# Kernel tuning notes

Hardware: AMD Instinct MI355X
Metric: run time of the kernel (lower is better)

Reference implementation:

```python
import jax, jax.numpy as jnp
import numpy as np

DIMS = [512, 256, 256, 256, 256, 256, 128, 128, 64, 40]
N_NODES = 100000
N_EDGES = 3200000


def setup_inputs() -> dict:
    key = jax.random.key(0)
    ks = jax.random.split(key, 4 + 2 * 9)
    inp = {
        "x": jax.random.normal(ks[0], (N_NODES, DIMS[0]), dtype=jnp.float32),
        "edge_src": jax.random.randint(ks[1], (N_EDGES,), 0, N_NODES, dtype=jnp.int32),
        "edge_dst": jax.random.randint(ks[2], (N_EDGES,), 0, N_NODES, dtype=jnp.int32),
        "edge_weight": jax.random.uniform(ks[3], (N_EDGES,), dtype=jnp.float32) / 32.0,
    }
    for i in range(9):
        fi, fo = DIMS[i], DIMS[i + 1]
        scale = 1.0 / np.sqrt(fi)
        inp[f"W{i+1}"] = jax.random.normal(ks[4 + 2 * i], (fi, fo), dtype=jnp.float32) * scale
        inp[f"b{i+1}"] = jax.random.normal(ks[5 + 2 * i], (fo,), dtype=jnp.float32) * scale
    return inp


def _gcn_layer(h, W, b, src, dst, w, n_nodes):
    # support = h @ W; out[i] = sum over edges (i <- j) of w * support[j] + b
    support = h @ W                          # [N, fo]
    msgs = w[:, None] * support[src]         # [E, fo] gather
    agg = jax.ops.segment_sum(msgs, dst, num_segments=n_nodes)  # [N, fo] scatter-add
    return agg + b


def reference(x, edge_src, edge_dst, edge_weight,
              W1, b1, W2, b2, W3, b3, W4, b4, W5, b5,
              W6, b6, W7, b7, W8, b8, W9, b9):
    n = x.shape[0]
    Ws = (W1, W2, W3, W4, W5, W6, W7, W8, W9)
    bs = (b1, b2, b3, b4, b5, b6, b7, b8, b9)
    h = x
    for i in range(8):  # layers 1..8 with ReLU
        h = jax.nn.relu(_gcn_layer(h, Ws[i], bs[i], edge_src, edge_dst, edge_weight, n))
    h = _gcn_layer(h, Ws[8], bs[8], edge_src, edge_dst, edge_weight, n)
    return jax.nn.log_softmax(h, axis=1)
```

## Files before the change

### kernel.cpp

```cpp
#include <hip/hip_runtime.h>
#include <cstdint>
#include <cstddef>

typedef __attribute__((ext_vector_type(8))) short bf16x8;
typedef __attribute__((ext_vector_type(4))) float f32x4;

static inline int cdiv(int a, int b) { return (a + b - 1) / b; }

__device__ inline unsigned short f2bf(float f) {
    union { float f; unsigned int u; } v; v.f = f;
    unsigned int u = v.u;
    return (unsigned short)((u + 0x7FFFu + ((u >> 16) & 1u)) >> 16);
}
__device__ inline float bf2f(unsigned short b) {
    union { unsigned int u; float f; } v; v.u = ((unsigned int)b) << 16;
    return v.f;
}

__device__ inline void fma16(float* a, const int4& d, float ws) {
    const int dw[4] = {d.x, d.y, d.z, d.w};
#pragma unroll
    for (int w = 0; w < 4; ++w) {
        a[w * 4 + 0] += ws * (float)(char)(dw[w]);
        a[w * 4 + 1] += ws * (float)(char)(dw[w] >> 8);
        a[w * 4 + 2] += ws * (float)(char)(dw[w] >> 16);
        a[w * 4 + 3] += ws * (float)(dw[w] >> 24);
    }
}


struct TW {
    const float* W[9];
    int K[9];
    int N[9];
    int base[10];
    int nN;
};

__global__ __launch_bounds__(256) void prep_kernel(TW tw, unsigned short* __restrict__ Wt,
                                                   int* __restrict__ deg,
                                                   int* __restrict__ bucketCursor, int total) {
    int t = blockIdx.x * 256 + threadIdx.x;
    if (t < tw.nN) deg[t] = 0;
    if (t < 8) bucketCursor[t] = 0;
    if (t >= total) return;
    int l = 0;
#pragma unroll
    for (int i = 1; i <= 8; ++i)
        if (t >= tw.base[i]) l = i;
    int loc = t - tw.base[l];
    int K = tw.K[l], N = tw.N[l];
    int n = loc / K, k = loc - n * K;
    float v = (n < N) ? tw.W[l][(size_t)k * N + n] : 0.f;
    Wt[t] = f2bf(v);
}


__global__ __launch_bounds__(256) void partition_kernel(
        const int* __restrict__ src, const int* __restrict__ dst,
        const float* __restrict__ w,
        int* __restrict__ bucketCursor, int4* __restrict__ staging,
        int bucketCap, int nE, int nN) {
    __shared__ int lcount[8];
    __shared__ int lbase[8];
    int tid = threadIdx.x;
    int i = blockIdx.x * 256 + tid;
    if (tid < 8) lcount[tid] = 0;
    __syncthreads();
    int b = 0, d = 0, s = 0, lslot = 0;
    float wv = 0.f;
    bool act = (i < nE);
    if (act) {
        d = dst[i]; s = src[i]; wv = w[i];
        b = (int)(((long long)d * 8) / nN);
        lslot = atomicAdd(&lcount[b], 1);
    }
    __syncthreads();
    if (tid < 8) lbase[tid] = lcount[tid] ? atomicAdd(&bucketCursor[tid], lcount[tid]) : 0;
    __syncthreads();
    if (act) {
        int pos = lbase[b] + lslot;
        staging[(size_t)b * bucketCap + pos] = make_int4(d, s, __float_as_int(wv), 0);
    }
}


#define DC_BPB 32

__global__ __launch_bounds__(256) void deg_count(const int4* __restrict__ staging,
                                                 const int* __restrict__ bucketCnt,
                                                 int bucketCap, int* __restrict__ deg, int nN) {
    __shared__ int hist[12512];
    int bucket = blockIdx.x & 7;
    int chunk = blockIdx.x >> 3;
    int cnt = bucketCnt[bucket];
    int lo = (int)(((long long)bucket * nN + 7) / 8);
    int hi = (int)(((long long)(bucket + 1) * nN + 7) / 8);
    if (hi > nN) hi = nN;
    int span = hi - lo;
    for (int i = threadIdx.x; i < span; i += 256) hist[i] = 0;
    __syncthreads();
    const int4* st = staging + (size_t)bucket * bucketCap;
    for (int i = chunk * 256 + threadIdx.x; i < cnt; i += DC_BPB * 256)
        atomicAdd(&hist[st[i].x - lo], 1);
    __syncthreads();
    for (int i = threadIdx.x; i < span; i += 256) {
        int v = hist[i];
        if (v) atomicAdd(&deg[lo + i], v);
    }
}


__global__ __launch_bounds__(256) void scan_part(const int* __restrict__ deg,
                                                 int* __restrict__ partials, int n) {
    __shared__ int sdata[256];
    int tid = threadIdx.x;
    int base = blockIdx.x * 1024;
    int local = 0;
#pragma unroll
    for (int i = 0; i < 4; ++i) {
        int idx = base + tid * 4 + i;
        local += (idx < n) ? deg[idx] : 0;
    }
    sdata[tid] = local;
    __syncthreads();
    for (int off = 128; off; off >>= 1) {
        if (tid < off) sdata[tid] += sdata[tid + off];
        __syncthreads();
    }
    if (tid == 0) partials[blockIdx.x] = sdata[0];
}

__global__ __launch_bounds__(256) void scan_final2(const int* __restrict__ deg,
                                                   const int* __restrict__ partials,
                                                   int* __restrict__ rowptr,
                                                   int* __restrict__ cursor, int n, int nb) {
    __shared__ int ps[128];
    __shared__ int sdata[256];
    int tid = threadIdx.x;
    if (tid < 128) ps[tid] = (tid < nb) ? partials[tid] : 0;
    __syncthreads();
    for (int off = 1; off < 128; off <<= 1) {
        int t = (tid < 128 && tid >= off) ? ps[tid - off] : 0;
        __syncthreads();
        if (tid < 128) ps[tid] += t;
        __syncthreads();
    }
    int base = (blockIdx.x == 0) ? 0 : ps[blockIdx.x - 1];
    if (blockIdx.x == 0 && tid == 0) rowptr[n] = ps[nb - 1];
    int bb = blockIdx.x * 1024;
    int vals[4];
    int local = 0;
#pragma unroll
    for (int i = 0; i < 4; ++i) {
        int idx = bb + tid * 4 + i;
        vals[i] = (idx < n) ? deg[idx] : 0;
        local += vals[i];
    }
    sdata[tid] = local;
    __syncthreads();
    for (int off = 1; off < 256; off <<= 1) {
        int t = (tid >= off) ? sdata[tid - off] : 0;
        __syncthreads();
        sdata[tid] += t;
        __syncthreads();
    }
    int run = sdata[tid] - local + base;
#pragma unroll
    for (int i = 0; i < 4; ++i) {
        int idx = bb + tid * 4 + i;
        if (idx < n) { rowptr[idx] = run; cursor[idx] = run; }
        run += vals[i];
    }
}


__global__ __launch_bounds__(256) void scatter_b(const int4* __restrict__ staging,
                                                 const int* __restrict__ bucketCnt,
                                                 int bucketCap, int* __restrict__ cursor,
                                                 int2* __restrict__ ep, int blocksPerBucket) {
    int bucket = blockIdx.x & 7;
    int chunk = blockIdx.x >> 3;
    int cnt = bucketCnt[bucket];
    const int4* st = staging + (size_t)bucket * bucketCap;
    for (int i = chunk * 256 + threadIdx.x; i < cnt; i += blocksPerBucket * 256) {
        int4 r = st[i];
        int pos = atomicAdd(&cursor[r.x], 1);
        ep[pos] = make_int2(r.y, r.z);
    }
}


template <int BN, bool AF32, bool OUTQ>
__global__ __launch_bounds__(256) void gemm_mfma(const void* __restrict__ Av,
                                                 const unsigned short* __restrict__ Bt,
                                                 void* __restrict__ Cv,
                                                 float* __restrict__ scArr,
                                                 int M, int K, int N) {
    constexpr int BM = 128, BK = 64;
    __shared__ unsigned short As[BM * BK];
    __shared__ unsigned short Bs[BN * BK];
    const int tid = threadIdx.x;
    const int lane = tid & 63, wid = tid >> 6;
    const int m0 = blockIdx.x * BM, n0 = blockIdx.y * BN;

    constexpr int WN = (BN == 128) ? 2 : 1;
    constexpr int WTM = (BN == 128) ? 64 : 32;
    constexpr int FM = WTM / 16, FN = 4;
    const int wm = (wid / WN) * WTM;
    const int wn = (wid % WN) * 64;
    const int g = lane >> 4, r16 = lane & 15;

    const unsigned short* A16 = (const unsigned short*)Av;
    const float* A32 = (const float*)Av;

    f32x4 acc[FM][FN] = {};

    for (int k0 = 0; k0 < K; k0 += BK) {
        if constexpr (AF32) {
#pragma unroll
            for (int it = 0; it < 4; ++it) {
                int c = it * 256 + tid;
                int r = c >> 3, kc = c & 7;
                int gm = m0 + r;
                bf16x8 val;
                if (gm < M) {
                    const float* p = A32 + (size_t)gm * K + k0 + kc * 8;
                    float4 v0 = *reinterpret_cast<const float4*>(p);
                    float4 v1 = *reinterpret_cast<const float4*>(p + 4);
                    val[0] = (short)f2bf(v0.x); val[1] = (short)f2bf(v0.y);
                    val[2] = (short)f2bf(v0.z); val[3] = (short)f2bf(v0.w);
                    val[4] = (short)f2bf(v1.x); val[5] = (short)f2bf(v1.y);
                    val[6] = (short)f2bf(v1.z); val[7] = (short)f2bf(v1.w);
                } else {
#pragma unroll
                    for (int j = 0; j < 8; ++j) val[j] = 0;
                }
                *reinterpret_cast<bf16x8*>(&As[r * BK + kc * 8]) = val;
            }
        } else {
#pragma unroll
            for (int c = 0; c < 4; ++c) {
                int base = wid * 32 + c * 8;
                int row = base + (lane >> 3), kc = lane & 7;
                const unsigned short* gp = A16 + (size_t)(m0 + row) * K + k0 + kc * 8;
                __builtin_amdgcn_global_load_lds(
                    (const __attribute__((address_space(1))) void*)gp,
                    (__attribute__((address_space(3))) void*)&As[base * BK], 16, 0, 0);
            }
        }
        {
            constexpr int BCALLS = (BN * BK) / (512 * 4);
#pragma unroll
            for (int c = 0; c < BCALLS; ++c) {
                int base = wid * (BN / 4) + c * 8;
                int row = base + (lane >> 3), kc = lane & 7;
                const unsigned short* gp = Bt + (size_t)(n0 + row) * K + k0 + kc * 8;
                __builtin_amdgcn_global_load_lds(
                    (const __attribute__((address_space(1))) void*)gp,
                    (__attribute__((address_space(3))) void*)&Bs[base * BK], 16, 0, 0);
            }
        }
        __syncthreads();
#pragma unroll
        for (int ks = 0; ks < 2; ++ks) {
            bf16x8 af[FM], bfr[FN];
#pragma unroll
            for (int i = 0; i < FM; ++i)
                af[i] = *reinterpret_cast<const bf16x8*>(&As[(wm + i * 16 + r16) * BK + ks * 32 + g * 8]);
#pragma unroll
            for (int j = 0; j < FN; ++j)
                bfr[j] = *reinterpret_cast<const bf16x8*>(&Bs[(wn + j * 16 + r16) * BK + ks * 32 + g * 8]);
#pragma unroll
            for (int i = 0; i < FM; ++i)
#pragma unroll
                for (int j = 0; j < FN; ++j)
                    acc[i][j] = __builtin_amdgcn_mfma_f32_16x16x32_bf16(af[i], bfr[j], acc[i][j], 0, 0, 0);
        }
        __syncthreads();
    }

    if constexpr (OUTQ) {
        __shared__ float rmax2[2][BM];
        const int wc = wid % WN;
        char* C8 = (char*)Cv;
#pragma unroll
        for (int i = 0; i < FM; ++i) {
#pragma unroll
            for (int r = 0; r < 4; ++r) {
                float m = 0.f;
#pragma unroll
                for (int j = 0; j < FN; ++j) m = fmaxf(m, fabsf(acc[i][j][r]));
                m = fmaxf(m, __shfl_xor(m, 1));
                m = fmaxf(m, __shfl_xor(m, 2));
                m = fmaxf(m, __shfl_xor(m, 4));
                m = fmaxf(m, __shfl_xor(m, 8));
                if (r16 == 0) rmax2[wc][wm + i * 16 + g * 4 + r] = m;
            }
        }
        __syncthreads();
#pragma unroll
        for (int i = 0; i < FM; ++i) {
#pragma unroll
            for (int r = 0; r < 4; ++r) {
                int rl = wm + i * 16 + g * 4 + r;
                float rm = fmaxf(rmax2[0][rl], rmax2[1][rl]);
                float inv = (rm > 0.f) ? 127.f / rm : 0.f;
                int gm = m0 + rl;
                if (gm < M) {
                    if (wc == 0 && r16 == 0)
                        scArr[(size_t)gm * 2 + blockIdx.y] = rm * (1.f / 127.f);
#pragma unroll
                    for (int j = 0; j < FN; ++j) {
                        int gn = n0 + wn + j * 16 + r16;
                        float q = fminf(fmaxf(rintf(acc[i][j][r] * inv), -127.f), 127.f);
                        C8[(size_t)gm * N + gn] = (char)(int)q;
                    }
                }
            }
        }
    } else {
        unsigned short* C = (unsigned short*)Cv;
#pragma unroll
        for (int i = 0; i < FM; ++i) {
            int gmBase = m0 + wm + i * 16 + g * 4;
#pragma unroll
            for (int j = 0; j < FN; ++j) {
                int gn = n0 + wn + j * 16 + r16;
                if (gn < N) {
#pragma unroll
                    for (int r = 0; r < 4; ++r) {
                        int gm = gmBase + r;
                        if (gm < M) C[(size_t)gm * N + gn] = f2bf(acc[i][j][r]);
                    }
                }
            }
        }
    }
}


template <int FO>
__global__ __launch_bounds__(256) void agg_q8(const char* __restrict__ supp8,
                                              const float* __restrict__ sc,
                                              const int2* __restrict__ ep,
                                              const int* __restrict__ rowptr,
                                              const float* __restrict__ bias,
                                              unsigned short* __restrict__ out, int n_nodes) {
    constexpr int LPR = FO / 16;
    constexpr int EPS = 64 / LPR;
    constexpr int G16 = 16 / EPS;
    constexpr int G8 = 8 / EPS;
    int node = (int)((blockIdx.x * blockDim.x + threadIdx.x) >> 6);
    int lane = threadIdx.x & 63;
    if (node >= n_nodes) return;
    int beg = __builtin_amdgcn_readfirstlane(rowptr[node]);
    int end = __builtin_amdgcn_readfirstlane(rowptr[node + 1]);
    const int lr = lane & (LPR - 1);
    const int half = lane / LPR;
    const int hi = (FO == 256) ? (lr >> 3) : 0;
    float a[16] = {};
    int e = beg;
    for (; e + 16 <= end; e += 16) {
        int2 me[G16];
#pragma unroll
        for (int u = 0; u < G16; ++u) me[u] = ep[e + u * EPS + half];
        float ss[G16];
        int4 q[G16];
#pragma unroll
        for (int u = 0; u < G16; ++u) ss[u] = sc[(size_t)me[u].x * 2 + hi];
#pragma unroll
        for (int u = 0; u < G16; ++u)
            q[u] = *reinterpret_cast<const int4*>(supp8 + (size_t)me[u].x * FO + lr * 16);
#pragma unroll
        for (int u = 0; u < G16; ++u)
            fma16(a, q[u], __int_as_float(me[u].y) * ss[u]);
    }
    for (; e + 8 <= end; e += 8) {
        int2 me[G8];
#pragma unroll
        for (int u = 0; u < G8; ++u) me[u] = ep[e + u * EPS + half];
        float ss[G8];
        int4 q[G8];
#pragma unroll
        for (int u = 0; u < G8; ++u) ss[u] = sc[(size_t)me[u].x * 2 + hi];
#pragma unroll
        for (int u = 0; u < G8; ++u)
            q[u] = *reinterpret_cast<const int4*>(supp8 + (size_t)me[u].x * FO + lr * 16);
#pragma unroll
        for (int u = 0; u < G8; ++u)
            fma16(a, q[u], __int_as_float(me[u].y) * ss[u]);
    }
    for (; e < end; ++e) {
        int2 me = ep[e];
        float ws = (half == 0) ? __int_as_float(me.y) * sc[(size_t)me.x * 2 + hi] : 0.f;
        int4 q = *reinterpret_cast<const int4*>(supp8 + (size_t)me.x * FO + lr * 16);
        fma16(a, q, ws);
    }
#pragma unroll
    for (int off = LPR; off < 64; off <<= 1)
#pragma unroll
        for (int j = 0; j < 16; ++j) a[j] += __shfl_xor(a[j], off);
    if (lane < LPR) {
        float bb[16];
#pragma unroll
        for (int c = 0; c < 4; ++c) {
            float4 bv = *reinterpret_cast<const float4*>(bias + lr * 16 + c * 4);
            bb[c * 4 + 0] = bv.x; bb[c * 4 + 1] = bv.y;
            bb[c * 4 + 2] = bv.z; bb[c * 4 + 3] = bv.w;
        }
        bf16x8 o0, o1;
#pragma unroll
        for (int j = 0; j < 8; ++j) {
            o0[j] = (short)f2bf(fmaxf(a[j] + bb[j], 0.f));
            o1[j] = (short)f2bf(fmaxf(a[j + 8] + bb[j + 8], 0.f));
        }
        unsigned short* op = out + (size_t)node * FO + lr * 16;
        *reinterpret_cast<bf16x8*>(op) = o0;
        *reinterpret_cast<bf16x8*>(op + 8) = o1;
    }
}


template <int FO>
__global__ __launch_bounds__(256) void agg_kernel(const unsigned short* __restrict__ supp,
                                                  const int2* __restrict__ ep,
                                                  const int* __restrict__ rowptr,
                                                  const float* __restrict__ bias,
                                                  unsigned short* __restrict__ out, int n_nodes) {
    constexpr int LPR = FO / 8;
    constexpr int EPS = 64 / LPR;
    constexpr int G16 = 16 / EPS;
    constexpr int G8 = 8 / EPS;
    int node = (int)((blockIdx.x * blockDim.x + threadIdx.x) >> 6);
    int lane = threadIdx.x & 63;
    if (node >= n_nodes) return;
    int beg = __builtin_amdgcn_readfirstlane(rowptr[node]);
    int end = __builtin_amdgcn_readfirstlane(rowptr[node + 1]);
    const int lr = lane & (LPR - 1);
    const int half = lane / LPR;
    float a[8] = {};
    int e = beg;
    for (; e + 16 <= end; e += 16) {
        int2 me[G16];
        bf16x8 v[G16];
#pragma unroll
        for (int u = 0; u < G16; ++u) me[u] = ep[e + u * EPS + half];
#pragma unroll
        for (int u = 0; u < G16; ++u)
            v[u] = *reinterpret_cast<const bf16x8*>(supp + (size_t)me[u].x * FO + lr * 8);
#pragma unroll
        for (int u = 0; u < G16; ++u) {
            float wv = __int_as_float(me[u].y);
#pragma unroll
            for (int j = 0; j < 8; ++j) a[j] += wv * bf2f((unsigned short)v[u][j]);
        }
    }
    for (; e + 8 <= end; e += 8) {
        int2 me[G8];
        bf16x8 v[G8];
#pragma unroll
        for (int u = 0; u < G8; ++u) me[u] = ep[e + u * EPS + half];
#pragma unroll
        for (int u = 0; u < G8; ++u)
            v[u] = *reinterpret_cast<const bf16x8*>(supp + (size_t)me[u].x * FO + lr * 8);
#pragma unroll
        for (int u = 0; u < G8; ++u) {
            float wv = __int_as_float(me[u].y);
#pragma unroll
            for (int j = 0; j < 8; ++j) a[j] += wv * bf2f((unsigned short)v[u][j]);
        }
    }
    for (; e < end; ++e) {
        int2 me = ep[e];
        bf16x8 v = *reinterpret_cast<const bf16x8*>(supp + (size_t)me.x * FO + lr * 8);
        float wv = (half == 0) ? __int_as_float(me.y) : 0.f;
#pragma unroll
        for (int j = 0; j < 8; ++j) a[j] += wv * bf2f((unsigned short)v[j]);
    }
#pragma unroll
    for (int off = LPR; off < 64; off <<= 1)
#pragma unroll
        for (int j = 0; j < 8; ++j) a[j] += __shfl_xor(a[j], off);
    if (lane < LPR) {
        float4 b0 = *reinterpret_cast<const float4*>(bias + lane * 8);
        float4 b1 = *reinterpret_cast<const float4*>(bias + lane * 8 + 4);
        float bb[8] = {b0.x, b0.y, b0.z, b0.w, b1.x, b1.y, b1.z, b1.w};
        bf16x8 o;
#pragma unroll
        for (int j = 0; j < 8; ++j) o[j] = (short)f2bf(fmaxf(a[j] + bb[j], 0.f));
        *reinterpret_cast<bf16x8*>(out + (size_t)node * FO + lane * 8) = o;
    }
}


__global__ __launch_bounds__(256) void agg_lsm_kernel(const unsigned short* __restrict__ supp,
                                                      const int2* __restrict__ ep,
                                                      const int* __restrict__ rowptr,
                                                      const float* __restrict__ bias,
                                                      float* __restrict__ out, int n_nodes) {
    int node = (int)((blockIdx.x * blockDim.x + threadIdx.x) >> 6);
    int lane = threadIdx.x & 63;
    if (node >= n_nodes) return;
    int beg = __builtin_amdgcn_readfirstlane(rowptr[node]);
    int end = __builtin_amdgcn_readfirstlane(rowptr[node + 1]);
    const int lr = lane & 7;
    const int half = lane >> 3;
    float a[8] = {};
    int e = beg;
    for (; e + 16 <= end; e += 16) {
        int2 me0 = ep[e + half];
        int2 me1 = ep[e + 8 + half];
        bf16x8 v0 = *reinterpret_cast<const bf16x8*>(supp + (size_t)me0.x * 64 + lr * 8);
        bf16x8 v1 = *reinterpret_cast<const bf16x8*>(supp + (size_t)me1.x * 64 + lr * 8);
        float w0 = __int_as_float(me0.y), w1 = __int_as_float(me1.y);
#pragma unroll
        for (int j = 0; j < 8; ++j)
            a[j] += w0 * bf2f((unsigned short)v0[j]) + w1 * bf2f((unsigned short)v1[j]);
    }
    for (; e + 8 <= end; e += 8) {
        int2 me = ep[e + half];
        bf16x8 v = *reinterpret_cast<const bf16x8*>(supp + (size_t)me.x * 64 + lr * 8);
        float wv = __int_as_float(me.y);
#pragma unroll
        for (int j = 0; j < 8; ++j) a[j] += wv * bf2f((unsigned short)v[j]);
    }
    for (; e < end; ++e) {
        int2 me = ep[e];
        bf16x8 v = *reinterpret_cast<const bf16x8*>(supp + (size_t)me.x * 64 + lr * 8);
        float wv = (half == 0) ? __int_as_float(me.y) : 0.f;
#pragma unroll
        for (int j = 0; j < 8; ++j) a[j] += wv * bf2f((unsigned short)v[j]);
    }
#pragma unroll
    for (int off = 8; off < 64; off <<= 1)
#pragma unroll
        for (int j = 0; j < 8; ++j) a[j] += __shfl_xor(a[j], off);
    float vj[8];
#pragma unroll
    for (int j = 0; j < 8; ++j) {
        int col = lane * 8 + j;
        float bv = (lane < 8 && col < 40) ? bias[col] : 0.f;
        vj[j] = (col < 40) ? (a[j] + bv) : -1e30f;
    }
    float m = vj[0];
#pragma unroll
    for (int j = 1; j < 8; ++j) m = fmaxf(m, vj[j]);
#pragma unroll
    for (int off = 1; off < 8; off <<= 1) m = fmaxf(m, __shfl_xor(m, off));
    float s = 0.f;
#pragma unroll
    for (int j = 0; j < 8; ++j) s += expf(vj[j] - m);
#pragma unroll
    for (int off = 1; off < 8; off <<= 1) s += __shfl_xor(s, off);
    float ls = m + logf(s);
    if (lane < 5) {
        float4 o0, o1;
        o0.x = vj[0] - ls; o0.y = vj[1] - ls; o0.z = vj[2] - ls; o0.w = vj[3] - ls;
        o1.x = vj[4] - ls; o1.y = vj[5] - ls; o1.z = vj[6] - ls; o1.w = vj[7] - ls;
        float* op = out + (size_t)node * 40 + lane * 8;
        *reinterpret_cast<float4*>(op) = o0;
        *reinterpret_cast<float4*>(op + 4) = o1;
    }
}


extern "C" void kernel_launch(void* const* d_in, const int* in_sizes, int n_in,
                              void* d_out, int out_size, void* d_ws, size_t ws_size,
                              hipStream_t stream) {
    const float* x    = (const float*)d_in[0];
    const int*   esrc = (const int*)d_in[1];
    const int*   edst = (const int*)d_in[2];
    const float* ew   = (const float*)d_in[3];

    const int nN = in_sizes[0] / 512;
    const int nE = in_sizes[1];

    const int dims[10] = {512, 256, 256, 256, 256, 256, 128, 128, 64, 40};
    const int BUCKET_CAP = ((nE / 8) + (nE / 64) + 4095) & ~4095;

    char* ws = (char*)d_ws;
    unsigned short* h    = (unsigned short*)ws;
    unsigned short* supp = (unsigned short*)(ws + (size_t)nN * 256 * 2);
    char* supp8 = (char*)supp;
    char* p = ws + (size_t)nN * 256 * 2 * 2;
    unsigned short* Wt = (unsigned short*)p; p += (1 << 21);
    float* scArr  = (float*)p; p += (size_t)nN * 2 * 4 + 256;
    int4* staging = (int4*)p; p += (size_t)8 * BUCKET_CAP * 16;
    int* deg      = (int*)p; p += ((size_t)nN + 64) * 4;
    int* rowptr   = (int*)p; p += ((size_t)nN + 64) * 4;
    int* cursor   = (int*)p; p += ((size_t)nN + 64) * 4;
    int* partials = (int*)p; p += 128 * 4;
    int* bucketCursor = (int*)p; p += 64 * 4;
    int2* ep      = (int2*)p; p += (size_t)nE * 8;

    TW tw;
    size_t woff[9];
    {
        int off = 0;
        for (int i = 0; i < 9; ++i) {
            tw.W[i] = (const float*)d_in[4 + 2 * i];
            tw.K[i] = dims[i];
            tw.N[i] = dims[i + 1];
            tw.base[i] = off;
            woff[i] = (size_t)off;
            int fop = cdiv(dims[i + 1], 64) * 64;
            off += fop * dims[i];
        }
        tw.base[9] = off;
        tw.nN = nN;
        int total = off;
        int nPrep = cdiv((total > nN + 8) ? total : nN + 8, 256);
        prep_kernel<<<nPrep, 256, 0, stream>>>(tw, Wt, deg, bucketCursor, total);
    }
    const float* b[9];
    for (int i = 0; i < 9; ++i) b[i] = (const float*)d_in[5 + 2 * i];

    partition_kernel<<<cdiv(nE, 256), 256, 0, stream>>>(esrc, edst, ew, bucketCursor,
                                                        staging, BUCKET_CAP, nE, nN);
    deg_count<<<8 * DC_BPB, 256, 0, stream>>>(staging, bucketCursor, BUCKET_CAP, deg, nN);
    {
        int nb = cdiv(nN, 1024);
        scan_part<<<nb, 256, 0, stream>>>(deg, partials, nN);
        scan_final2<<<nb, 256, 0, stream>>>(deg, partials, rowptr, cursor, nN, nb);
    }
    scatter_b<<<8 * 256, 256, 0, stream>>>(staging, bucketCursor, BUCKET_CAP, cursor, ep, 256);

    const int aggBlocks = cdiv(nN, 4);
    const int gBlocks = cdiv(nN, 128);

    const void* A = (const void*)x;
    for (int L = 0; L < 9; ++L) {
        int fi = dims[L], fo = dims[L + 1];
        if (L == 8) {
            dim3 g(gBlocks, 1);
            gemm_mfma<64, false, false><<<g, 256, 0, stream>>>(A, Wt + woff[L], (void*)supp,
                                                               scArr, nN, fi, 64);
            agg_lsm_kernel<<<aggBlocks, 256, 0, stream>>>(supp, ep, rowptr, b[8], (float*)d_out, nN);
            break;
        }
        if (fo == 256) {
            dim3 g(gBlocks, 2);
            if (L == 0)
                gemm_mfma<128, true, true><<<g, 256, 0, stream>>>(A, Wt + woff[L], (void*)supp8,
                                                                  scArr, nN, fi, fo);
            else
                gemm_mfma<128, false, true><<<g, 256, 0, stream>>>(A, Wt + woff[L], (void*)supp8,
                                                                   scArr, nN, fi, fo);
            agg_q8<256><<<aggBlocks, 256, 0, stream>>>(supp8, scArr, ep, rowptr, b[L], h, nN);
        } else if (fo == 128) {
            dim3 g(gBlocks, 1);
            gemm_mfma<128, false, true><<<g, 256, 0, stream>>>(A, Wt + woff[L], (void*)supp8,
                                                               scArr, nN, fi, fo);
            agg_q8<128><<<aggBlocks, 256, 0, stream>>>(supp8, scArr, ep, rowptr, b[L], h, nN);
        } else {
            dim3 g(gBlocks, 1);
            gemm_mfma<64, false, false><<<g, 256, 0, stream>>>(A, Wt + woff[L], (void*)supp,
                                                               scArr, nN, fi, fo);
            agg_kernel<64><<<aggBlocks, 256, 0, stream>>>(supp, ep, rowptr, b[L], h, nN);
        }
        A = (const void*)h;
    }
}
```

Measured before the change: 1.866 ms.

## Use offset-binary int8 support with bias correction and quantize the 64-wide layer

Int8 support values are now stored offset by 128 as unsigned bytes, so unpacking needs only a mask and convert instead of sign extension. The aggregation subtracts 128 times the running sum of edge weights to undo the offset. Layer 8 (fo=64) now uses a new quantized GEMM epilogue and agg_q8<64> in place of the bf16 path, halving its gather bytes. Tail loops in agg_q8 and agg_lsm are replaced by one predicated vector pass. The offset correction can add rounding error, and the new 64-wide path carries extra per-row quantization error.

```diff
diff --git a/kernel.cpp b/kernel.cpp
--- a/kernel.cpp
+++ b/kernel.cpp
@@ -17,13 +17,13 @@
     return v.f;
 }
 
-__device__ inline void fma16(float* a, const int4& d, float ws) {
-    const int dw[4] = {d.x, d.y, d.z, d.w};
+__device__ inline void fma16u(float* a, const int4& d, float ws) {
+    const unsigned int dw[4] = {(unsigned)d.x, (unsigned)d.y, (unsigned)d.z, (unsigned)d.w};
 #pragma unroll
     for (int w = 0; w < 4; ++w) {
-        a[w * 4 + 0] += ws * (float)(char)(dw[w]);
-        a[w * 4 + 1] += ws * (float)(char)(dw[w] >> 8);
-        a[w * 4 + 2] += ws * (float)(char)(dw[w] >> 16);
+        a[w * 4 + 0] += ws * (float)(dw[w] & 0xFFu);
+        a[w * 4 + 1] += ws * (float)((dw[w] >> 8) & 0xFFu);
+        a[w * 4 + 2] += ws * (float)((dw[w] >> 16) & 0xFFu);
         a[w * 4 + 3] += ws * (float)(dw[w] >> 24);
     }
 }
@@ -191,7 +191,7 @@
 }
 
 
-template <int BN, bool AF32, bool OUTQ>
+template <int BN, bool AF32, int OUTQ>
 __global__ __launch_bounds__(256) void gemm_mfma(const void* __restrict__ Av,
                                                  const unsigned short* __restrict__ Bt,
                                                  void* __restrict__ Cv,
@@ -280,10 +280,10 @@
         __syncthreads();
     }
 
-    if constexpr (OUTQ) {
+    if constexpr (OUTQ == 1) {
         __shared__ float rmax2[2][BM];
         const int wc = wid % WN;
-        char* C8 = (char*)Cv;
+        unsigned char* C8 = (unsigned char*)Cv;
 #pragma unroll
         for (int i = 0; i < FM; ++i) {
 #pragma unroll
@@ -314,7 +314,33 @@
                     for (int j = 0; j < FN; ++j) {
                         int gn = n0 + wn + j * 16 + r16;
                         float q = fminf(fmaxf(rintf(acc[i][j][r] * inv), -127.f), 127.f);
-                        C8[(size_t)gm * N + gn] = (char)(int)q;
+                        C8[(size_t)gm * N + gn] = (unsigned char)((int)q + 128);
+                    }
+                }
+            }
+        }
+    } else if constexpr (OUTQ == 2) {
+        unsigned char* C8 = (unsigned char*)Cv;
+#pragma unroll
+        for (int i = 0; i < FM; ++i) {
+#pragma unroll
+            for (int r = 0; r < 4; ++r) {
+                float m = 0.f;
+#pragma unroll
+                for (int j = 0; j < FN; ++j) m = fmaxf(m, fabsf(acc[i][j][r]));
+                m = fmaxf(m, __shfl_xor(m, 1));
+                m = fmaxf(m, __shfl_xor(m, 2));
+                m = fmaxf(m, __shfl_xor(m, 4));
+                m = fmaxf(m, __shfl_xor(m, 8));
+                float inv = (m > 0.f) ? 127.f / m : 0.f;
+                int gm = m0 + wm + i * 16 + g * 4 + r;
+                if (gm < M) {
+                    if (r16 == 0) scArr[(size_t)gm * 2] = m * (1.f / 127.f);
+#pragma unroll
+                    for (int j = 0; j < FN; ++j) {
+                        int gn = wn + j * 16 + r16;
+                        float q = fminf(fmaxf(rintf(acc[i][j][r] * inv), -127.f), 127.f);
+                        C8[(size_t)gm * 64 + gn] = (unsigned char)((int)q + 128);
                     }
                 }
             }
@@ -351,6 +377,7 @@
     constexpr int EPS = 64 / LPR;
     constexpr int G16 = 16 / EPS;
     constexpr int G8 = 8 / EPS;
+    constexpr int TG = (FO == 256) ? 2 : 1;
     int node = (int)((blockIdx.x * blockDim.x + threadIdx.x) >> 6);
     int lane = threadIdx.x & 63;
     if (node >= n_nodes) return;
@@ -360,6 +387,7 @@
     const int half = lane / LPR;
     const int hi = (FO == 256) ? (lr >> 3) : 0;
     float a[16] = {};
+    float wsum = 0.f;
     int e = beg;
     for (; e + 16 <= end; e += 16) {
         int2 me[G16];
@@ -373,30 +401,49 @@
         for (int u = 0; u < G16; ++u)
             q[u] = *reinterpret_cast<const int4*>(supp8 + (size_t)me[u].x * FO + lr * 16);
 #pragma unroll
-        for (int u = 0; u < G16; ++u)
-            fma16(a, q[u], __int_as_float(me[u].y) * ss[u]);
-    }
-    for (; e + 8 <= end; e += 8) {
-        int2 me[G8];
-#pragma unroll
-        for (int u = 0; u < G8; ++u) me[u] = ep[e + u * EPS + half];
-        float ss[G8];
-        int4 q[G8];
-#pragma unroll
-        for (int u = 0; u < G8; ++u) ss[u] = sc[(size_t)me[u].x * 2 + hi];
-#pragma unroll
-        for (int u = 0; u < G8; ++u)
-            q[u] = *reinterpret_cast<const int4*>(supp8 + (size_t)me[u].x * FO + lr * 16);
-#pragma unroll
-        for (int u = 0; u < G8; ++u)
-            fma16(a, q[u], __int_as_float(me[u].y) * ss[u]);
-    }
-    for (; e < end; ++e) {
-        int2 me = ep[e];
-        float ws = (half == 0) ? __int_as_float(me.y) * sc[(size_t)me.x * 2 + hi] : 0.f;
-        int4 q = *reinterpret_cast<const int4*>(supp8 + (size_t)me.x * FO + lr * 16);
-        fma16(a, q, ws);
-    }
+        for (int u = 0; u < G16; ++u) {
+            float ws = __int_as_float(me[u].y) * ss[u];
+            fma16u(a, q[u], ws);
+            wsum += ws;
+        }
+    }
+    if constexpr (G8 >= 1) {
+        for (; e + 8 <= end; e += 8) {
+            int2 me[G8];
+#pragma unroll
+            for (int u = 0; u < G8; ++u) me[u] = ep[e + u * EPS + half];
+            float ss[G8];
+            int4 q[G8];
+#pragma unroll
+            for (int u = 0; u < G8; ++u) ss[u] = sc[(size_t)me[u].x * 2 + hi];
+#pragma unroll
+            for (int u = 0; u < G8; ++u)
+                q[u] = *reinterpret_cast<const int4*>(supp8 + (size_t)me[u].x * FO + lr * 16);
+#pragma unroll
+            for (int u = 0; u < G8; ++u) {
+                float ws = __int_as_float(me[u].y) * ss[u];
+                fma16u(a, q[u], ws);
+                wsum += ws;
+            }
+        }
+    }
+    {
+        int rem = end - e;
+        if (rem > 0) {
+#pragma unroll
+            for (int u = 0; u < TG; ++u) {
+                int idx = u * EPS + half;
+                bool ok = idx < rem;
+                int2 me = ep[e + (ok ? idx : 0)];
+                float ws = ok ? __int_as_float(me.y) * sc[(size_t)me.x * 2 + hi] : 0.f;
+                int4 q = *reinterpret_cast<const int4*>(supp8 + (size_t)me.x * FO + lr * 16);
+                fma16u(a, q, ws);
+                wsum += ws;
+            }
+        }
+    }
+#pragma unroll
+    for (int j = 0; j < 16; ++j) a[j] -= 128.f * wsum;
 #pragma unroll
     for (int off = LPR; off < 64; off <<= 1)
 #pragma unroll
@@ -418,78 +465,6 @@
         unsigned short* op = out + (size_t)node * FO + lr * 16;
         *reinterpret_cast<bf16x8*>(op) = o0;
         *reinterpret_cast<bf16x8*>(op + 8) = o1;
-    }
-}
-
-
-template <int FO>
-__global__ __launch_bounds__(256) void agg_kernel(const unsigned short* __restrict__ supp,
-                                                  const int2* __restrict__ ep,
-                                                  const int* __restrict__ rowptr,
-                                                  const float* __restrict__ bias,
-                                                  unsigned short* __restrict__ out, int n_nodes) {
-    constexpr int LPR = FO / 8;
-    constexpr int EPS = 64 / LPR;
-    constexpr int G16 = 16 / EPS;
-    constexpr int G8 = 8 / EPS;
-    int node = (int)((blockIdx.x * blockDim.x + threadIdx.x) >> 6);
-    int lane = threadIdx.x & 63;
-    if (node >= n_nodes) return;
-    int beg = __builtin_amdgcn_readfirstlane(rowptr[node]);
-    int end = __builtin_amdgcn_readfirstlane(rowptr[node + 1]);
-    const int lr = lane & (LPR - 1);
-    const int half = lane / LPR;
-    float a[8] = {};
-    int e = beg;
-    for (; e + 16 <= end; e += 16) {
-        int2 me[G16];
-        bf16x8 v[G16];
-#pragma unroll
-        for (int u = 0; u < G16; ++u) me[u] = ep[e + u * EPS + half];
-#pragma unroll
-        for (int u = 0; u < G16; ++u)
-            v[u] = *reinterpret_cast<const bf16x8*>(supp + (size_t)me[u].x * FO + lr * 8);
-#pragma unroll
-        for (int u = 0; u < G16; ++u) {
-            float wv = __int_as_float(me[u].y);
-#pragma unroll
-            for (int j = 0; j < 8; ++j) a[j] += wv * bf2f((unsigned short)v[u][j]);
-        }
-    }
-    for (; e + 8 <= end; e += 8) {
-        int2 me[G8];
-        bf16x8 v[G8];
-#pragma unroll
-        for (int u = 0; u < G8; ++u) me[u] = ep[e + u * EPS + half];
-#pragma unroll
-        for (int u = 0; u < G8; ++u)
-            v[u] = *reinterpret_cast<const bf16x8*>(supp + (size_t)me[u].x * FO + lr * 8);
-#pragma unroll
-        for (int u = 0; u < G8; ++u) {
-            float wv = __int_as_float(me[u].y);
-#pragma unroll
-            for (int j = 0; j < 8; ++j) a[j] += wv * bf2f((unsigned short)v[u][j]);
-        }
-    }
-    for (; e < end; ++e) {
-        int2 me = ep[e];
-        bf16x8 v = *reinterpret_cast<const bf16x8*>(supp + (size_t)me.x * FO + lr * 8);
-        float wv = (half == 0) ? __int_as_float(me.y) : 0.f;
-#pragma unroll
-        for (int j = 0; j < 8; ++j) a[j] += wv * bf2f((unsigned short)v[j]);
-    }
-#pragma unroll
-    for (int off = LPR; off < 64; off <<= 1)
-#pragma unroll
-        for (int j = 0; j < 8; ++j) a[j] += __shfl_xor(a[j], off);
-    if (lane < LPR) {
-        float4 b0 = *reinterpret_cast<const float4*>(bias + lane * 8);
-        float4 b1 = *reinterpret_cast<const float4*>(bias + lane * 8 + 4);
-        float bb[8] = {b0.x, b0.y, b0.z, b0.w, b1.x, b1.y, b1.z, b1.w};
-        bf16x8 o;
-#pragma unroll
-        for (int j = 0; j < 8; ++j) o[j] = (short)f2bf(fmaxf(a[j] + bb[j], 0.f));
-        *reinterpret_cast<bf16x8*>(out + (size_t)node * FO + lane * 8) = o;
     }
 }
 
@@ -518,19 +493,20 @@
         for (int j = 0; j < 8; ++j)
             a[j] += w0 * bf2f((unsigned short)v0[j]) + w1 * bf2f((unsigned short)v1[j]);
     }
-    for (; e + 8 <= end; e += 8) {
-        int2 me = ep[e + half];
-        bf16x8 v = *reinterpret_cast<const bf16x8*>(supp + (size_t)me.x * 64 + lr * 8);
-        float wv = __int_as_float(me.y);
-#pragma unroll
-        for (int j = 0; j < 8; ++j) a[j] += wv * bf2f((unsigned short)v[j]);
-    }
-    for (; e < end; ++e) {
-        int2 me = ep[e];
-        bf16x8 v = *reinterpret_cast<const bf16x8*>(supp + (size_t)me.x * 64 + lr * 8);
-        float wv = (half == 0) ? __int_as_float(me.y) : 0.f;
-#pragma unroll
-        for (int j = 0; j < 8; ++j) a[j] += wv * bf2f((unsigned short)v[j]);
+    {
+        int rem = end - e;
+        if (rem > 0) {
+#pragma unroll
+            for (int u = 0; u < 2; ++u) {
+                int idx = u * 8 + half;
+                bool ok = idx < rem;
+                int2 me = ep[e + (ok ? idx : 0)];
+                float wv = ok ? __int_as_float(me.y) : 0.f;
+                bf16x8 v = *reinterpret_cast<const bf16x8*>(supp + (size_t)me.x * 64 + lr * 8);
+#pragma unroll
+                for (int j = 0; j < 8; ++j) a[j] += wv * bf2f((unsigned short)v[j]);
+            }
+        }
     }
 #pragma unroll
     for (int off = 8; off < 64; off <<= 1)
@@ -634,30 +610,30 @@
         int fi = dims[L], fo = dims[L + 1];
         if (L == 8) {
             dim3 g(gBlocks, 1);
-            gemm_mfma<64, false, false><<<g, 256, 0, stream>>>(A, Wt + woff[L], (void*)supp,
-                                                               scArr, nN, fi, 64);
+            gemm_mfma<64, false, 0><<<g, 256, 0, stream>>>(A, Wt + woff[L], (void*)supp,
+                                                           scArr, nN, fi, 64);
             agg_lsm_kernel<<<aggBlocks, 256, 0, stream>>>(supp, ep, rowptr, b[8], (float*)d_out, nN);
             break;
         }
         if (fo == 256) {
             dim3 g(gBlocks, 2);
             if (L == 0)
-                gemm_mfma<128, true, true><<<g, 256, 0, stream>>>(A, Wt + woff[L], (void*)supp8,
-                                                                  scArr, nN, fi, fo);
+                gemm_mfma<128, true, 1><<<g, 256, 0, stream>>>(A, Wt + woff[L], (void*)supp8,
+                                                               scArr, nN, fi, fo);
             else
-                gemm_mfma<128, false, true><<<g, 256, 0, stream>>>(A, Wt + woff[L], (void*)supp8,
-                                                                   scArr, nN, fi, fo);
+                gemm_mfma<128, false, 1><<<g, 256, 0, stream>>>(A, Wt + woff[L], (void*)supp8,
+                                                                scArr, nN, fi, fo);
             agg_q8<256><<<aggBlocks, 256, 0, stream>>>(supp8, scArr, ep, rowptr, b[L], h, nN);
         } else if (fo == 128) {
             dim3 g(gBlocks, 1);
-            gemm_mfma<128, false, true><<<g, 256, 0, stream>>>(A, Wt + woff[L], (void*)supp8,
-                                                               scArr, nN, fi, fo);
+            gemm_mfma<128, false, 1><<<g, 256, 0, stream>>>(A, Wt + woff[L], (void*)supp8,
+                                                            scArr, nN, fi, fo);
             agg_q8<128><<<aggBlocks, 256, 0, stream>>>(supp8, scArr, ep, rowptr, b[L], h, nN);
         } else {
             dim3 g(gBlocks, 1);
-            gemm_mfma<64, false, false><<<g, 256, 0, stream>>>(A, Wt + woff[L], (void*)supp,
-                                                               scArr, nN, fi, fo);
-            agg_kernel<64><<<aggBlocks, 256, 0, stream>>>(supp, ep, rowptr, b[L], h, nN);
+            gemm_mfma<64, false, 2><<<g, 256, 0, stream>>>(A, Wt + woff[L], (void*)supp8,
+                                                           scArr, nN, fi, fo);
+            agg_q8<64><<<aggBlocks, 256, 0, stream>>>(supp8, scArr, ep, rowptr, b[L], h, nN);
         }
         A = (const void*)h;
     }
```

Result: faster. 1.727 ms (-7.4%).
